# Kernel optimization log

Measured on AMD Instinct MI355X. Metric: run time of the kernel, lower is better.

Reference implementation:

```python
import jax, jax.numpy as jnp
import numpy as np

B, L = 256, 65536
HIST, WIN = 256, 64
DIM, NPAT = 256, 64
AMP = 2.0


def setup_inputs() -> dict:
    key = jax.random.key(0)
    k1, k2, k3, k4, k5, k6 = jax.random.split(key, 6)
    x = jax.random.uniform(k1, (B, L), dtype=jnp.float32)
    avg = jax.random.uniform(k2, (B, NPAT), dtype=jnp.float32)
    avg_scores = avg - avg.mean(axis=-1, keepdims=True)
    # conv kernel (out=dim, in=1, k=history), kaiming-ish scale
    conv_w = jax.random.normal(k3, (DIM, 1, HIST), dtype=jnp.float32) * (1.0 / np.sqrt(HIST))
    conv_b = jax.random.normal(k4, (DIM,), dtype=jnp.float32) * 0.01
    # xavier-uniform keys
    lim = np.sqrt(6.0 / (DIM + NPAT))
    keys = jax.random.uniform(k5, (DIM, NPAT), minval=-lim, maxval=lim, dtype=jnp.float32)
    # shapes ~ rand * amp * 2 in [0, 4]
    shapes = jax.random.uniform(k6, (NPAT, WIN), dtype=jnp.float32) * (AMP * 2.0)
    return {"x": x, "avg_scores": avg_scores, "conv_w": conv_w, "conv_b": conv_b,
            "keys": keys, "shapes": shapes}


def reference(x, avg_scores, conv_w, conv_b, keys, shapes):
    batch, seqlen = x.shape
    n_pat = keys.shape[1]
    # Conv1d(1, dim, history, stride=window) on left-padded input, then ReLU
    # (dropout is identity at inference)
    out = jax.lax.conv_general_dilated(
        x[:, None, :], conv_w,
        window_strides=(WIN,), padding=[(HIST - 1, 0)],
        dimension_numbers=("NCH", "OIH", "NCH"))  # (B, dim, T)
    out = jax.nn.relu(out + conv_b[None, :, None])
    out = jnp.transpose(out, (2, 0, 1))  # (T, B, dim)
    # relu6(out @ keys): (T, B, n_patterns)
    attn_scores = jnp.clip(jnp.einsum("tbd,dp->tbp", out, keys), 0.0, 6.0)

    inv_p = 1.0 / n_pat

    def step(avg, score):  # avg, score: (B, n_patterns)
        prob = jax.nn.softmax(score - avg, axis=-1)
        return avg + prob - inv_p, prob

    _, probs = jax.lax.scan(step, avg_scores, attn_scores)  # probs: (T, B, P)
    attn_probs = jnp.transpose(probs, (1, 0, 2))  # (B, T, P)
    signal = jnp.einsum("btp,pw->btw", attn_probs, shapes).reshape(batch, -1)[:, :seqlen]
    return jax.nn.relu(signal - x)
```

## Files before the change

### kernel.cpp

```cpp
#include <hip/hip_runtime.h>

#define BB 256
#define LL 65536
#define TS 1024
#define HIST 256
#define WINW 64
#define DIM 256
#define NPAT 64

typedef short s8v __attribute__((ext_vector_type(8)));
typedef float f4v __attribute__((ext_vector_type(4)));

#define MFMA16(a, b, c) __builtin_amdgcn_mfma_f32_16x16x32_bf16((a), (b), (c), 0, 0, 0)
#define LOG2E 1.44269504f

__device__ __forceinline__ short bf16rne(float f) {
    unsigned u = __float_as_uint(f);
    unsigned r = (u + 0x7fffu + ((u >> 16) & 1u)) >> 16;
    return (short)r;
}
__device__ __forceinline__ float bf16tof(short h) {
    return __uint_as_float(((unsigned)(unsigned short)h) << 16);
}
__device__ __forceinline__ void split2(float f, short& hi, short& lo) {
    hi = bf16rne(f);
    lo = bf16rne(f - bf16tof(hi));
}

__global__ void prep_all(const float* __restrict__ w, short* __restrict__ wFH,
                         short* __restrict__ wFL,
                         const float* __restrict__ keys, short* __restrict__ kFH,
                         short* __restrict__ kFL,
                         const float* __restrict__ sh, short* __restrict__ sFH,
                         short* __restrict__ sFL) {
    int bid = blockIdx.x;
    s8v hv, lv;
    if (bid < 32) {
        int idx = bid * 256 + threadIdx.x;
        int d = idx & 255, qk = idx >> 8;
        int h0 = qk * 8;
#pragma unroll
        for (int j = 0; j < 8; ++j) {
            short h, l; split2(w[d * HIST + h0 + j], h, l);
            hv[j] = h; lv[j] = l;
        }
        *(s8v*)(wFH + (size_t)idx * 8) = hv;
        *(s8v*)(wFL + (size_t)idx * 8) = lv;
    } else if (bid < 40) {
        int idx = (bid - 32) * 256 + threadIdx.x;
        int p = idx & 63, qk = idx >> 6;
        int d0 = qk * 8;
#pragma unroll
        for (int j = 0; j < 8; ++j) {
            short h, l; split2(keys[(d0 + j) * NPAT + p], h, l);
            hv[j] = h; lv[j] = l;
        }
        *(s8v*)(kFH + (size_t)idx * 8) = hv;
        *(s8v*)(kFL + (size_t)idx * 8) = lv;
    } else {
        int idx = (bid - 40) * 256 + threadIdx.x;
        int ww = idx & 63, qk = idx >> 6;
        int p0 = qk * 8;
#pragma unroll
        for (int j = 0; j < 8; ++j) {
            short h, l; split2(sh[(p0 + j) * WINW + ww], h, l);
            hv[j] = h; lv[j] = l;
        }
        *(s8v*)(sFH + (size_t)idx * 8) = hv;
        *(s8v*)(sFL + (size_t)idx * 8) = lv;
    }
}

#define WELEM 2240
#define WUNIT 280
#define HPAD 264

__device__ __forceinline__ int swz(int u) { return u ^ ((u >> 3) & 7); }

__launch_bounds__(256, 2)
__global__ void scores_mfma(const float* __restrict__ x,
                            const short* __restrict__ wFH, const short* __restrict__ wFL,
                            const short* __restrict__ kFH, const short* __restrict__ kFL,
                            const float* __restrict__ conv_b,
                            float* __restrict__ scoresT) {
    __shared__ __align__(16) short xsH[WUNIT * 8], xsL[WUNIT * 8];
    __shared__ __align__(16) short hidH[32 * HPAD], hidL[32 * HPAD];

    const int b = blockIdx.y, t0 = blockIdx.x * 32;
    const int tid = threadIdx.x;
    const int lane = tid & 63, wid = tid >> 6;
    const int m = lane & 15, q = lane >> 4;

    const float* xb = x + (size_t)b * LL;
    const int gbase = t0 * WINW - (HIST - 1);
    for (int i = tid; i < WELEM; i += 256) {
        int gi = gbase + i;
        float v = (gi >= 0) ? xb[gi] : 0.0f;
        short h, l; split2(v, h, l);
        int pos = (swz(i >> 3) << 3) | (i & 7);
        xsH[pos] = h; xsL[pos] = l;
    }
    __syncthreads();

    const int nb = wid * 64;
    f4v acc[2][4];
#pragma unroll
    for (int mt = 0; mt < 2; ++mt)
#pragma unroll
        for (int nt = 0; nt < 4; ++nt) acc[mt][nt] = (f4v)0.0f;

    for (int kt = 0; kt < 8; ++kt) {
        s8v aH[2], aL[2];
#pragma unroll
        for (int mt = 0; mt < 2; ++mt) {
            int row = mt * 16 + m;
            int su = swz(row * 8 + kt * 4 + q) << 3;
            aH[mt] = *(const s8v*)&xsH[su];
            aL[mt] = *(const s8v*)&xsL[su];
        }
        s8v bH[4], bL[4];
#pragma unroll
        for (int nt = 0; nt < 4; ++nt) {
            size_t bi = ((size_t)(kt * 4 + q) * 256 + nb + nt * 16 + m) * 8;
            bH[nt] = *(const s8v*)(wFH + bi);
            bL[nt] = *(const s8v*)(wFL + bi);
        }
#pragma unroll
        for (int mt = 0; mt < 2; ++mt)
#pragma unroll
            for (int nt = 0; nt < 4; ++nt) {
                acc[mt][nt] = MFMA16(aH[mt], bH[nt], acc[mt][nt]);
                acc[mt][nt] = MFMA16(aL[mt], bH[nt], acc[mt][nt]);
                acc[mt][nt] = MFMA16(aH[mt], bL[nt], acc[mt][nt]);
            }
    }

#pragma unroll
    for (int mt = 0; mt < 2; ++mt)
#pragma unroll
        for (int nt = 0; nt < 4; ++nt) {
            int d = nb + nt * 16 + m;
            float bias = conv_b[d];
#pragma unroll
            for (int r = 0; r < 4; ++r) {
                int row = mt * 16 + q * 4 + r;
                float v = fmaxf(acc[mt][nt][r] + bias, 0.0f);
                short h, l; split2(v, h, l);
                hidH[row * HPAD + d] = h;
                hidL[row * HPAD + d] = l;
            }
        }
    __syncthreads();

    const int pb = wid * 16;
    f4v acc2[2];
    acc2[0] = (f4v)0.0f; acc2[1] = (f4v)0.0f;
    for (int kt = 0; kt < 8; ++kt) {
        s8v aH[2], aL[2];
#pragma unroll
        for (int mt = 0; mt < 2; ++mt) {
            int off = (mt * 16 + m) * HPAD + kt * 32 + q * 8;
            aH[mt] = *(const s8v*)&hidH[off];
            aL[mt] = *(const s8v*)&hidL[off];
        }
        size_t bi = ((size_t)(kt * 4 + q) * 64 + pb + m) * 8;
        s8v bH = *(const s8v*)(kFH + bi);
        s8v bL = *(const s8v*)(kFL + bi);
#pragma unroll
        for (int mt = 0; mt < 2; ++mt) {
            acc2[mt] = MFMA16(aH[mt], bH, acc2[mt]);
            acc2[mt] = MFMA16(aL[mt], bH, acc2[mt]);
            acc2[mt] = MFMA16(aH[mt], bL, acc2[mt]);
        }
    }
#pragma unroll
    for (int mt = 0; mt < 2; ++mt) {
        float4 st;
        st.x = fminf(fmaxf(acc2[mt][0], 0.0f), 6.0f) * LOG2E;
        st.y = fminf(fmaxf(acc2[mt][1], 0.0f), 6.0f) * LOG2E;
        st.z = fminf(fmaxf(acc2[mt][2], 0.0f), 6.0f) * LOG2E;
        st.w = fminf(fmaxf(acc2[mt][3], 0.0f), 6.0f) * LOG2E;
        *(float4*)&scoresT[((size_t)b * NPAT + pb + m) * TS + t0 + mt * 16 + q * 4] = st;
    }
}

template <int CTRL>
__device__ __forceinline__ float dppadd(float x) {
    int t = __builtin_amdgcn_update_dpp(0, __float_as_int(x), CTRL, 0xf, 0xf, true);
    return x + __int_as_float(t);
}

__launch_bounds__(64)
__global__ void scan_kernel(const float* __restrict__ scoresT,
                            const float* __restrict__ avg0,
                            float* __restrict__ probsT) {
    const int blk = blockIdx.x;
    const int bA = 2 * blk, bB = 2 * blk + 1;
    const int p = threadIdx.x;

    const float4* sA = (const float4*)(scoresT + ((size_t)bA * NPAT + p) * TS);
    const float4* sB = (const float4*)(scoresT + ((size_t)bB * NPAT + p) * TS);
    float4* qA = (float4*)(probsT + ((size_t)bA * NPAT + p) * TS);
    float4* qB = (float4*)(probsT + ((size_t)bB * NPAT + p) * TS);

    float avgA = avg0[bA * NPAT + p] * LOG2E;
    float avgB = avg0[bB * NPAT + p] * LOG2E;
    const float invc = LOG2E / NPAT;

    float4 bufA[4], bufB[4];
#pragma unroll
    for (int s = 0; s < 4; ++s) { bufA[s] = sA[s]; bufB[s] = sB[s]; }

    for (int base = 0; base < TS / 4; base += 4) {
#pragma unroll
        for (int s = 0; s < 4; ++s) {
            const int g = base + s;
            float4 vA = bufA[s], vB = bufB[s];
            float4 prA, prB;
            float* a = (float*)&vA;  float* bv = (float*)&vB;
            float* pa = (float*)&prA; float* pb = (float*)&prB;
#pragma unroll
            for (int j = 0; j < 4; ++j) {
                float eA = exp2f(a[j] - avgA);
                float eB = exp2f(bv[j] - avgB);
                float wA = eA, wB = eB;
                wA = dppadd<0x111>(wA); wB = dppadd<0x111>(wB);
                wA = dppadd<0x112>(wA); wB = dppadd<0x112>(wB);
                wA = dppadd<0x114>(wA); wB = dppadd<0x114>(wB);
                wA = dppadd<0x118>(wA); wB = dppadd<0x118>(wB);
                wA = dppadd<0x142>(wA); wB = dppadd<0x142>(wB);
                wA = dppadd<0x143>(wA); wB = dppadd<0x143>(wB);
                float tA = __int_as_float(__builtin_amdgcn_readlane(__float_as_int(wA), 63));
                float tB = __int_as_float(__builtin_amdgcn_readlane(__float_as_int(wB), 63));
                float prAv = eA * __builtin_amdgcn_rcpf(tA);
                float prBv = eB * __builtin_amdgcn_rcpf(tB);
                pa[j] = prAv; pb[j] = prBv;
                avgA = __builtin_fmaf(prAv, LOG2E, avgA - invc);
                avgB = __builtin_fmaf(prBv, LOG2E, avgB - invc);
            }
            if (g + 4 < TS / 4) {
                bufA[s] = sA[g + 4];
                bufB[s] = sB[g + 4];
            }
            qA[g] = prA;
            qB[g] = prB;
        }
    }
}

__launch_bounds__(256)
__global__ void signal_mfma(const float* __restrict__ probsT,
                            const short* __restrict__ sFH, const short* __restrict__ sFL,
                            const float* __restrict__ x,
                            float* __restrict__ out) {
    __shared__ __align__(16) short pH[64 * 72], pL[64 * 72];
    const int b = blockIdx.y, t0 = blockIdx.x * 64;
    const int tid = threadIdx.x;
    const int lane = tid & 63, wid = tid >> 6;
    const int m = lane & 15, q = lane >> 4;

    {
        const int pl = tid & 63, ck = tid >> 6;
        const float* src = probsT + ((size_t)b * NPAT + pl) * TS + t0 + ck * 16;
#pragma unroll
        for (int k = 0; k < 4; ++k) {
            float4 v = *(const float4*)(src + k * 4);
            float* vp = (float*)&v;
#pragma unroll
            for (int j = 0; j < 4; ++j) {
                short h, l; split2(vp[j], h, l);
                int t = ck * 16 + k * 4 + j;
                pH[t * 72 + pl] = h;
                pL[t * 72 + pl] = l;
            }
        }
    }
    __syncthreads();

    f4v acc[4];
#pragma unroll
    for (int nt = 0; nt < 4; ++nt) acc[nt] = (f4v)0.0f;

#pragma unroll
    for (int kt = 0; kt < 2; ++kt) {
        int off = (wid * 16 + m) * 72 + kt * 32 + q * 8;
        s8v aH = *(const s8v*)&pH[off];
        s8v aL = *(const s8v*)&pL[off];
#pragma unroll
        for (int nt = 0; nt < 4; ++nt) {
            size_t bi = ((size_t)(kt * 4 + q) * 64 + nt * 16 + m) * 8;
            s8v bH = *(const s8v*)(sFH + bi);
            s8v bL = *(const s8v*)(sFL + bi);
            acc[nt] = MFMA16(aH, bH, acc[nt]);
            acc[nt] = MFMA16(aL, bH, acc[nt]);
            acc[nt] = MFMA16(aH, bL, acc[nt]);
        }
    }
#pragma unroll
    for (int nt = 0; nt < 4; ++nt)
#pragma unroll
        for (int r = 0; r < 4; ++r) {
            int row = wid * 16 + q * 4 + r;
            int w = nt * 16 + m;
            size_t gi = (size_t)b * LL + (size_t)(t0 + row) * WINW + w;
            out[gi] = fmaxf(acc[nt][r] - x[gi], 0.0f);
        }
}

extern "C" void kernel_launch(void* const* d_in, const int* in_sizes, int n_in,
                              void* d_out, int out_size, void* d_ws, size_t ws_size,
                              hipStream_t stream) {
    const float* x      = (const float*)d_in[0];
    const float* avg0   = (const float*)d_in[1];
    const float* conv_w = (const float*)d_in[2];
    const float* conv_b = (const float*)d_in[3];
    const float* keys   = (const float*)d_in[4];
    const float* shapes = (const float*)d_in[5];
    float* out = (float*)d_out;

    char* ws = (char*)d_ws;
    size_t o = 0;
    float* scoresT = (float*)(ws + o); o += (size_t)BB * TS * NPAT * 4;
    float* probsT  = (float*)(ws + o); o += (size_t)BB * TS * NPAT * 4;
    short* wFH = (short*)(ws + o); o += 8192 * 16;
    short* wFL = (short*)(ws + o); o += 8192 * 16;
    short* kFH = (short*)(ws + o); o += 2048 * 16;
    short* kFL = (short*)(ws + o); o += 2048 * 16;
    short* sFH = (short*)(ws + o); o += 512 * 16;
    short* sFL = (short*)(ws + o); o += 512 * 16;

    prep_all<<<42, 256, 0, stream>>>(conv_w, wFH, wFL, keys, kFH, kFL, shapes, sFH, sFL);
    scores_mfma<<<dim3(TS / 32, BB), 256, 0, stream>>>(x, wFH, wFL, kFH, kFL, conv_b, scoresT);
    scan_kernel<<<dim3(BB / 2), 64, 0, stream>>>(scoresT, avg0, probsT);
    signal_mfma<<<dim3(TS / 64, BB), 256, 0, stream>>>(probsT, sFH, sFL, x, out);
}
```

Before: 449.1 us.

## Load conv input straight from global into MFMA fragments, drop LDS staging

The conv-phase x window is no longer staged in shared memory. Each lane reads aligned float4 pairs directly from global memory and splits them into bf16 hi/lo fragments, which needs a shifted weight layout (index offset by one) plus a separate FMA for the last tap. The hidden-tile shared buffer now uses an XOR swizzle instead of padding. Launch bounds allow 4 blocks per CU. This removes the staging loop and one barrier and raises occupancy, at the cost of redundant global reads of x across waves and extra register pressure.

```diff
diff --git a/kernel.cpp b/kernel.cpp
--- a/kernel.cpp
+++ b/kernel.cpp
@@ -38,10 +38,12 @@
     if (bid < 32) {
         int idx = bid * 256 + threadIdx.x;
         int d = idx & 255, qk = idx >> 8;
-        int h0 = qk * 8;
+        int h0 = qk * 8 - 1;
 #pragma unroll
         for (int j = 0; j < 8; ++j) {
-            short h, l; split2(w[d * HIST + h0 + j], h, l);
+            int hh = h0 + j;
+            float wv = (hh >= 0) ? w[d * HIST + hh] : 0.0f;
+            short h, l; split2(wv, h, l);
             hv[j] = h; lv[j] = l;
         }
         *(s8v*)(wFH + (size_t)idx * 8) = hv;
@@ -71,20 +73,62 @@
     }
 }
 
-#define WELEM 2240
-#define WUNIT 280
-#define HPAD 264
-
-__device__ __forceinline__ int swz(int u) { return u ^ ((u >> 3) & 7); }
-
-__launch_bounds__(256, 2)
+template <bool EDGE>
+__device__ __forceinline__ void conv_phase(const float* __restrict__ xb, int gbase,
+                                           int m, int q, int nb,
+                                           const short* __restrict__ wFH,
+                                           const short* __restrict__ wFL,
+                                           f4v acc[2][4]) {
+    for (int kt = 0; kt < 8; ++kt) {
+        s8v aH[2], aL[2];
+#pragma unroll
+        for (int mt = 0; mt < 2; ++mt) {
+            const int g0 = gbase + (mt * 16 + m) * WINW + kt * 32 + q * 8;
+            float v[8];
+            if (EDGE) {
+#pragma unroll
+                for (int j = 0; j < 8; ++j) {
+                    int gi = g0 + j;
+                    v[j] = (gi >= 0) ? xb[gi] : 0.0f;
+                }
+            } else {
+                f4v u0 = *(const f4v*)(xb + g0);
+                f4v u1 = *(const f4v*)(xb + g0 + 4);
+#pragma unroll
+                for (int j = 0; j < 4; ++j) { v[j] = u0[j]; v[j + 4] = u1[j]; }
+            }
+#pragma unroll
+            for (int j = 0; j < 8; ++j) {
+                short h, l; split2(v[j], h, l);
+                aH[mt][j] = h; aL[mt][j] = l;
+            }
+        }
+        s8v bH[4], bL[4];
+#pragma unroll
+        for (int nt = 0; nt < 4; ++nt) {
+            size_t bi = ((size_t)(kt * 4 + q) * 256 + nb + nt * 16 + m) * 8;
+            bH[nt] = *(const s8v*)(wFH + bi);
+            bL[nt] = *(const s8v*)(wFL + bi);
+        }
+#pragma unroll
+        for (int mt = 0; mt < 2; ++mt)
+#pragma unroll
+            for (int nt = 0; nt < 4; ++nt) {
+                acc[mt][nt] = MFMA16(aH[mt], bH[nt], acc[mt][nt]);
+                acc[mt][nt] = MFMA16(aL[mt], bH[nt], acc[mt][nt]);
+                acc[mt][nt] = MFMA16(aH[mt], bL[nt], acc[mt][nt]);
+            }
+    }
+}
+
+__launch_bounds__(256, 4)
 __global__ void scores_mfma(const float* __restrict__ x,
                             const short* __restrict__ wFH, const short* __restrict__ wFL,
                             const short* __restrict__ kFH, const short* __restrict__ kFL,
+                            const float* __restrict__ conv_w,
                             const float* __restrict__ conv_b,
                             float* __restrict__ scoresT) {
-    __shared__ __align__(16) short xsH[WUNIT * 8], xsL[WUNIT * 8];
-    __shared__ __align__(16) short hidH[32 * HPAD], hidL[32 * HPAD];
+    __shared__ __align__(16) short hidH[32 * 256], hidL[32 * 256];
 
     const int b = blockIdx.y, t0 = blockIdx.x * 32;
     const int tid = threadIdx.x;
@@ -92,48 +136,26 @@
     const int m = lane & 15, q = lane >> 4;
 
     const float* xb = x + (size_t)b * LL;
-    const int gbase = t0 * WINW - (HIST - 1);
-    for (int i = tid; i < WELEM; i += 256) {
-        int gi = gbase + i;
-        float v = (gi >= 0) ? xb[gi] : 0.0f;
-        short h, l; split2(v, h, l);
-        int pos = (swz(i >> 3) << 3) | (i & 7);
-        xsH[pos] = h; xsL[pos] = l;
-    }
-    __syncthreads();
-
+    const int gbase = t0 * WINW - HIST;
     const int nb = wid * 64;
+
     f4v acc[2][4];
 #pragma unroll
     for (int mt = 0; mt < 2; ++mt)
 #pragma unroll
         for (int nt = 0; nt < 4; ++nt) acc[mt][nt] = (f4v)0.0f;
 
-    for (int kt = 0; kt < 8; ++kt) {
-        s8v aH[2], aL[2];
-#pragma unroll
-        for (int mt = 0; mt < 2; ++mt) {
-            int row = mt * 16 + m;
-            int su = swz(row * 8 + kt * 4 + q) << 3;
-            aH[mt] = *(const s8v*)&xsH[su];
-            aL[mt] = *(const s8v*)&xsL[su];
-        }
-        s8v bH[4], bL[4];
-#pragma unroll
-        for (int nt = 0; nt < 4; ++nt) {
-            size_t bi = ((size_t)(kt * 4 + q) * 256 + nb + nt * 16 + m) * 8;
-            bH[nt] = *(const s8v*)(wFH + bi);
-            bL[nt] = *(const s8v*)(wFL + bi);
-        }
-#pragma unroll
-        for (int mt = 0; mt < 2; ++mt)
-#pragma unroll
-            for (int nt = 0; nt < 4; ++nt) {
-                acc[mt][nt] = MFMA16(aH[mt], bH[nt], acc[mt][nt]);
-                acc[mt][nt] = MFMA16(aL[mt], bH[nt], acc[mt][nt]);
-                acc[mt][nt] = MFMA16(aH[mt], bL[nt], acc[mt][nt]);
-            }
-    }
+    if (t0 == 0)
+        conv_phase<true>(xb, gbase, m, q, nb, wFH, wFL, acc);
+    else
+        conv_phase<false>(xb, gbase, m, q, nb, wFH, wFL, acc);
+
+    float xv[2][4];
+#pragma unroll
+    for (int mt = 0; mt < 2; ++mt)
+#pragma unroll
+        for (int r = 0; r < 4; ++r)
+            xv[mt][r] = xb[(size_t)(t0 + mt * 16 + q * 4 + r) * WINW];
 
 #pragma unroll
     for (int mt = 0; mt < 2; ++mt)
@@ -141,25 +163,28 @@
         for (int nt = 0; nt < 4; ++nt) {
             int d = nb + nt * 16 + m;
             float bias = conv_b[d];
+            float w255 = conv_w[d * HIST + 255];
 #pragma unroll
             for (int r = 0; r < 4; ++r) {
                 int row = mt * 16 + q * 4 + r;
-                float v = fmaxf(acc[mt][nt][r] + bias, 0.0f);
+                float v = fmaxf(__builtin_fmaf(xv[mt][r], w255, acc[mt][nt][r] + bias), 0.0f);
                 short h, l; split2(v, h, l);
-                hidH[row * HPAD + d] = h;
-                hidL[row * HPAD + d] = l;
+                int dd = d ^ ((row & 7) << 3);
+                hidH[row * 256 + dd] = h;
+                hidL[row * 256 + dd] = l;
             }
         }
     __syncthreads();
 
     const int pb = wid * 16;
+    const int sw0 = (m & 7) << 3;
     f4v acc2[2];
     acc2[0] = (f4v)0.0f; acc2[1] = (f4v)0.0f;
     for (int kt = 0; kt < 8; ++kt) {
         s8v aH[2], aL[2];
 #pragma unroll
         for (int mt = 0; mt < 2; ++mt) {
-            int off = (mt * 16 + m) * HPAD + kt * 32 + q * 8;
+            int off = (mt * 16 + m) * 256 + ((kt * 32 + q * 8) ^ sw0);
             aH[mt] = *(const s8v*)&hidH[off];
             aL[mt] = *(const s8v*)&hidL[off];
         }
@@ -330,7 +355,8 @@
     short* sFL = (short*)(ws + o); o += 512 * 16;
 
     prep_all<<<42, 256, 0, stream>>>(conv_w, wFH, wFL, keys, kFH, kFL, shapes, sFH, sFL);
-    scores_mfma<<<dim3(TS / 32, BB), 256, 0, stream>>>(x, wFH, wFL, kFH, kFL, conv_b, scoresT);
+    scores_mfma<<<dim3(TS / 32, BB), 256, 0, stream>>>(x, wFH, wFL, kFH, kFL, conv_w,
+                                                       conv_b, scoresT);
     scan_kernel<<<dim3(BB / 2), 64, 0, stream>>>(scoresT, avg0, probsT);
     signal_mfma<<<dim3(TS / 64, BB), 256, 0, stream>>>(probsT, sFH, sFL, x, out);
 }
```

Measured after the change: 615.6 us. +37.1%, slower.

## Alias conv input tile with hidden buffer, swizzle hidden LDS, raise occupancy

Applied to the files above, without the earlier changes.

Reuses one shared buffer for the input window and the hidden activations, separated by an added barrier, and drops padding in favour of an XOR swizzle. This cuts LDS per block so the launch bound can request 4 blocks per CU. The MFMA chains are reordered so dependent accumulations are interleaved, and the second GEMM uses three separate accumulators to break the serial dependency. The risks are register pressure under the tighter launch bound and the cost of the extra barrier.

```diff
diff --git a/kernel.cpp b/kernel.cpp
--- a/kernel.cpp
+++ b/kernel.cpp
@@ -73,18 +73,18 @@
 
 #define WELEM 2240
 #define WUNIT 280
-#define HPAD 264
 
 __device__ __forceinline__ int swz(int u) { return u ^ ((u >> 3) & 7); }
 
-__launch_bounds__(256, 2)
+__launch_bounds__(256, 4)
 __global__ void scores_mfma(const float* __restrict__ x,
                             const short* __restrict__ wFH, const short* __restrict__ wFL,
                             const short* __restrict__ kFH, const short* __restrict__ kFL,
                             const float* __restrict__ conv_b,
                             float* __restrict__ scoresT) {
-    __shared__ __align__(16) short xsH[WUNIT * 8], xsL[WUNIT * 8];
-    __shared__ __align__(16) short hidH[32 * HPAD], hidL[32 * HPAD];
+    __shared__ __align__(16) short hidH[32 * 256], hidL[32 * 256];
+    short* xsH = hidH;
+    short* xsL = hidL;
 
     const int b = blockIdx.y, t0 = blockIdx.x * 32;
     const int tid = threadIdx.x;
@@ -128,12 +128,20 @@
 #pragma unroll
         for (int mt = 0; mt < 2; ++mt)
 #pragma unroll
-            for (int nt = 0; nt < 4; ++nt) {
+            for (int nt = 0; nt < 4; ++nt)
                 acc[mt][nt] = MFMA16(aH[mt], bH[nt], acc[mt][nt]);
+#pragma unroll
+        for (int mt = 0; mt < 2; ++mt)
+#pragma unroll
+            for (int nt = 0; nt < 4; ++nt)
                 acc[mt][nt] = MFMA16(aL[mt], bH[nt], acc[mt][nt]);
+#pragma unroll
+        for (int mt = 0; mt < 2; ++mt)
+#pragma unroll
+            for (int nt = 0; nt < 4; ++nt)
                 acc[mt][nt] = MFMA16(aH[mt], bL[nt], acc[mt][nt]);
-            }
-    }
+    }
+    __syncthreads();
 
 #pragma unroll
     for (int mt = 0; mt < 2; ++mt)
@@ -146,20 +154,25 @@
                 int row = mt * 16 + q * 4 + r;
                 float v = fmaxf(acc[mt][nt][r] + bias, 0.0f);
                 short h, l; split2(v, h, l);
-                hidH[row * HPAD + d] = h;
-                hidL[row * HPAD + d] = l;
+                int dd = d ^ ((row & 7) << 3);
+                hidH[row * 256 + dd] = h;
+                hidL[row * 256 + dd] = l;
             }
         }
     __syncthreads();
 
     const int pb = wid * 16;
-    f4v acc2[2];
-    acc2[0] = (f4v)0.0f; acc2[1] = (f4v)0.0f;
+    const int sw0 = (m & 7) << 3;
+    f4v aHH[2], aLH[2], aHL[2];
+#pragma unroll
+    for (int mt = 0; mt < 2; ++mt) {
+        aHH[mt] = (f4v)0.0f; aLH[mt] = (f4v)0.0f; aHL[mt] = (f4v)0.0f;
+    }
     for (int kt = 0; kt < 8; ++kt) {
         s8v aH[2], aL[2];
 #pragma unroll
         for (int mt = 0; mt < 2; ++mt) {
-            int off = (mt * 16 + m) * HPAD + kt * 32 + q * 8;
+            int off = (mt * 16 + m) * 256 + ((kt * 32 + q * 8) ^ sw0);
             aH[mt] = *(const s8v*)&hidH[off];
             aL[mt] = *(const s8v*)&hidL[off];
         }
@@ -167,19 +180,23 @@
         s8v bH = *(const s8v*)(kFH + bi);
         s8v bL = *(const s8v*)(kFL + bi);
 #pragma unroll
-        for (int mt = 0; mt < 2; ++mt) {
-            acc2[mt] = MFMA16(aH[mt], bH, acc2[mt]);
-            acc2[mt] = MFMA16(aL[mt], bH, acc2[mt]);
-            acc2[mt] = MFMA16(aH[mt], bL, acc2[mt]);
-        }
+        for (int mt = 0; mt < 2; ++mt)
+            aHH[mt] = MFMA16(aH[mt], bH, aHH[mt]);
+#pragma unroll
+        for (int mt = 0; mt < 2; ++mt)
+            aLH[mt] = MFMA16(aL[mt], bH, aLH[mt]);
+#pragma unroll
+        for (int mt = 0; mt < 2; ++mt)
+            aHL[mt] = MFMA16(aH[mt], bL, aHL[mt]);
     }
 #pragma unroll
     for (int mt = 0; mt < 2; ++mt) {
+        f4v s = aHH[mt] + aLH[mt] + aHL[mt];
         float4 st;
-        st.x = fminf(fmaxf(acc2[mt][0], 0.0f), 6.0f) * LOG2E;
-        st.y = fminf(fmaxf(acc2[mt][1], 0.0f), 6.0f) * LOG2E;
-        st.z = fminf(fmaxf(acc2[mt][2], 0.0f), 6.0f) * LOG2E;
-        st.w = fminf(fmaxf(acc2[mt][3], 0.0f), 6.0f) * LOG2E;
+        st.x = fminf(fmaxf(s[0], 0.0f), 6.0f) * LOG2E;
+        st.y = fminf(fmaxf(s[1], 0.0f), 6.0f) * LOG2E;
+        st.z = fminf(fmaxf(s[2], 0.0f), 6.0f) * LOG2E;
+        st.w = fminf(fmaxf(s[3], 0.0f), 6.0f) * LOG2E;
         *(float4*)&scoresT[((size_t)b * NPAT + pb + m) * TS + t0 + mt * 16 + q * 4] = st;
     }
 }
```

Measured after the change: 416.8 us. 1.08x faster.
